# Kernel tuning notes

Measured on AMD Instinct MI355X. Metric: run time of the kernel, lower is better.

## Reference

```python
import jax, jax.numpy as jnp
import numpy as np

NEG_SLOPE = 0.2  # PyG GATConv default negative_slope


def _add_self_loops(edge_index, num_nodes):
    # PyG GATConv add_self_loops=True default
    loop = jnp.arange(num_nodes, dtype=edge_index.dtype)
    src = jnp.concatenate([edge_index[0], loop])
    dst = jnp.concatenate([edge_index[1], loop])
    return src, dst


def _gat_layer(x, src, dst, W, att_src, att_dst, bias, heads, out_ch):
    """One PyG-style GATConv layer (concat=True).
    x: [N, F_in]; W: [F_in, heads*out_ch]; att_*: [heads, out_ch]; bias: [heads*out_ch].
    """
    N = x.shape[0]
    h = (x @ W).reshape(N, heads, out_ch)               # [N, H, C]
    a_src = jnp.einsum('nhc,hc->nh', h, att_src)        # [N, H]
    a_dst = jnp.einsum('nhc,hc->nh', h, att_dst)        # [N, H]
    logits = jax.nn.leaky_relu(a_src[src] + a_dst[dst], NEG_SLOPE)  # [E, H]
    # segment softmax over destination neighborhoods
    m = jax.ops.segment_max(logits, dst, num_segments=N)            # [N, H]
    e = jnp.exp(logits - m[dst])                                     # [E, H]
    s = jax.ops.segment_sum(e, dst, num_segments=N)                  # [N, H]
    alpha = e / s[dst]                                               # [E, H]
    # scatter-aggregate weighted source features
    out = jax.ops.segment_sum(alpha[:, :, None] * h[src], dst, num_segments=N)  # [N, H, C]
    return out.reshape(N, heads * out_ch) + bias


def setup_inputs() -> dict:
    key = jax.random.key(0)
    ks = jax.random.split(key, 10)
    N, E = 50000, 800000
    F_in, HID, H, NC = 128, 64, 4, 10
    x = jax.random.normal(ks[0], (N, F_in), dtype=jnp.float32)
    edge_index = jax.random.randint(ks[1], (2, E), 0, N, dtype=jnp.int64)
    sc1 = 1.0 / np.sqrt(F_in)
    sc2 = 1.0 / np.sqrt(HID * H)
    return {
        'x': x,
        'edge_index': edge_index,
        'W1': jax.random.normal(ks[2], (F_in, H * HID), dtype=jnp.float32) * sc1,
        'att_src1': jax.random.normal(ks[3], (H, HID), dtype=jnp.float32) * sc1,
        'att_dst1': jax.random.normal(ks[4], (H, HID), dtype=jnp.float32) * sc1,
        'b1': jnp.zeros((H * HID,), dtype=jnp.float32),
        'W2': jax.random.normal(ks[5], (H * HID, NC), dtype=jnp.float32) * sc2,
        'att_src2': jax.random.normal(ks[6], (1, NC), dtype=jnp.float32) * sc2,
        'att_dst2': jax.random.normal(ks[7], (1, NC), dtype=jnp.float32) * sc2,
        'b2': jnp.zeros((NC,), dtype=jnp.float32),
    }


def reference(x, edge_index, W1, att_src1, att_dst1, b1, W2, att_src2, att_dst2, b2):
    N = x.shape[0]
    src, dst = _add_self_loops(edge_index, N)
    h = _gat_layer(x, src, dst, W1, att_src1, att_dst1, b1, heads=4, out_ch=64)
    h = jax.nn.elu(h)
    out = _gat_layer(h, src, dst, W2, att_src2, att_dst2, b2, heads=1, out_ch=10)
    return out
```

## Files before the change

kernel.cpp:

```cpp
#include <hip/hip_runtime.h>
#include <hip/hip_fp16.h>
#include <math.h>

#define NEG_SLOPE 0.2f
#define LOG2E 1.44269504088896f

#if __has_builtin(__builtin_amdgcn_exp2f)
#define EXP2(x) __builtin_amdgcn_exp2f(x)
#else
#define EXP2(x) exp2f(x)
#endif

typedef _Float16 half8 __attribute__((ext_vector_type(8)));
typedef float floatx4 __attribute__((ext_vector_type(4)));

#define SRC_TILE_SHIFT 13
#define NTILES 8

__global__ __launch_bounds__(256) void prep1(const float* __restrict__ W1,
                                             half8* __restrict__ Bpack,
                                             int* __restrict__ deg, int N) {
  if (blockIdx.x < 16) {
    int tid = blockIdx.x * 256 + threadIdx.x;
    int l = tid & 63;
    int ksnt = tid >> 6;
    int ks = ksnt & 3;
    int nt = ksnt >> 2;
    int col = nt * 16 + (l & 15);
    int krow = ks * 32 + (l >> 4) * 8;
    half8 v;
#pragma unroll
    for (int j = 0; j < 8; j++) v[j] = (_Float16)W1[(krow + j) * 256 + col];
    Bpack[tid] = v;
  } else {
    int i = (blockIdx.x - 16) * 256 + threadIdx.x;
    if (i < N * NTILES) deg[i] = 0;
  }
}

__global__ __launch_bounds__(256) void phase2(
    const float* __restrict__ x, const half8* __restrict__ Bpack,
    const float* __restrict__ att_s, const float* __restrict__ att_d,
    unsigned char* __restrict__ h1q, float* __restrict__ a1sx,
    float* __restrict__ a1d,
    const int* __restrict__ src, const int* __restrict__ dst,
    int* __restrict__ deg, int* __restrict__ rank,
    int N, int E, int gemmBlocks, int histBlocks) {
  if ((int)blockIdx.x >= gemmBlocks) {
    int b = blockIdx.x - gemmBlocks;
    for (int e = b * 256 + threadIdx.x; e < E; e += histBlocks * 256) {
      int tile = src[e] >> SRC_TILE_SHIFT;
      rank[e] = atomicAdd(deg + dst[e] * NTILES + tile, 1);
    }
    return;
  }
  const int wave = threadIdx.x >> 6, lane = threadIdx.x & 63;
  const int quad = lane >> 4, li = lane & 15;
  const int n0 = (blockIdx.x * 4 + wave) * 16;
  if (n0 >= N) return;
  floatx4 acc[16];
#pragma unroll
  for (int t = 0; t < 16; t++) acc[t] = (floatx4){0.f, 0.f, 0.f, 0.f};
  const float* xrow = x + (size_t)(n0 + li) * 128;
#pragma unroll
  for (int ks = 0; ks < 4; ks++) {
    float4 xa = *(const float4*)(xrow + ks * 32 + quad * 8);
    float4 xb = *(const float4*)(xrow + ks * 32 + quad * 8 + 4);
    half8 a;
    a[0] = (_Float16)xa.x; a[1] = (_Float16)xa.y;
    a[2] = (_Float16)xa.z; a[3] = (_Float16)xa.w;
    a[4] = (_Float16)xb.x; a[5] = (_Float16)xb.y;
    a[6] = (_Float16)xb.z; a[7] = (_Float16)xb.w;
#pragma unroll
    for (int nt = 0; nt < 16; nt++) {
      half8 b = Bpack[(nt * 4 + ks) * 64 + lane];
      acc[nt] = __builtin_amdgcn_mfma_f32_16x16x32_f16(a, b, acc[nt], 0, 0, 0);
    }
  }
#pragma unroll
  for (int r = 0; r < 4; r++) {
    float m = 0.f;
#pragma unroll
    for (int nt = 0; nt < 16; nt++) m = fmaxf(m, fabsf(acc[nt][r]));
#pragma unroll
    for (int off = 8; off > 0; off >>= 1) m = fmaxf(m, __shfl_xor(m, off, 16));
    m = fmaxf(m, 1e-8f);
    float inv = 127.0f / m;
    int node = n0 + quad * 4 + r;
    if (li == 0) a1sx[(size_t)node * 8 + 4] = m * (1.0f / 127.0f);
#pragma unroll
    for (int nt = 0; nt < 16; nt++) {
      h1q[(size_t)node * 256 + nt * 16 + li] =
          (unsigned char)(int)(fmaf(acc[nt][r], inv, 128.5f));
    }
  }
  float as_f[16], ad_f[16];
#pragma unroll
  for (int nt = 0; nt < 16; nt++) {
    as_f[nt] = att_s[nt * 16 + li];
    ad_f[nt] = att_d[nt * 16 + li];
  }
#pragma unroll
  for (int r = 0; r < 4; r++) {
    int node = n0 + quad * 4 + r;
#pragma unroll
    for (int h = 0; h < 4; h++) {
      float vs = 0.f, vd = 0.f;
#pragma unroll
      for (int ntl = 0; ntl < 4; ntl++) {
        int nt = h * 4 + ntl;
        vs = fmaf(acc[nt][r], as_f[nt], vs);
        vd = fmaf(acc[nt][r], ad_f[nt], vd);
      }
#pragma unroll
      for (int off = 8; off > 0; off >>= 1) {
        vs += __shfl_down(vs, off, 16);
        vd += __shfl_down(vd, off, 16);
      }
      if (li == 0) {
        a1sx[(size_t)node * 8 + h] = vs * LOG2E;
        a1d[node * 4 + h] = vd * LOG2E;
      }
    }
  }
}

__global__ void scan_local(const int* __restrict__ deg, int* __restrict__ excl,
                           int* __restrict__ bsum, int N) {
  __shared__ int s[256];
  int i = blockIdx.x * 256 + threadIdx.x;
  int v = 0;
  if (i < N) {
    const int4* dp = (const int4*)(deg + (size_t)i * NTILES);
    int4 c0 = dp[0], c1 = dp[1];
    v = c0.x + c0.y + c0.z + c0.w + c1.x + c1.y + c1.z + c1.w + 1;
  }
  s[threadIdx.x] = v;
  __syncthreads();
  for (int off = 1; off < 256; off <<= 1) {
    int t = (threadIdx.x >= off) ? s[threadIdx.x - off] : 0;
    __syncthreads();
    s[threadIdx.x] += t;
    __syncthreads();
  }
  if (i < N) excl[i] = s[threadIdx.x] - v;
  if (threadIdx.x == 255) bsum[blockIdx.x] = s[255];
}

__global__ void scan_add2(const int* __restrict__ excl, const int* __restrict__ bsum,
                          int* __restrict__ rowptr, int* __restrict__ elist,
                          int N, int nb) {
  __shared__ int s[256];
  int v = (threadIdx.x < nb) ? bsum[threadIdx.x] : 0;
  s[threadIdx.x] = v;
  __syncthreads();
  for (int off = 1; off < 256; off <<= 1) {
    int t = (threadIdx.x >= off) ? s[threadIdx.x - off] : 0;
    __syncthreads();
    s[threadIdx.x] += t;
    __syncthreads();
  }
  __syncthreads();
  int base = (blockIdx.x > 0) ? s[blockIdx.x - 1] : 0;
  int i = blockIdx.x * 256 + threadIdx.x;
  if (i < N) {
    int r = excl[i] + base;
    rowptr[i] = r;
    elist[r] = i;
  }
  if (blockIdx.x == 0 && threadIdx.x == 0) rowptr[N] = s[nb - 1];
}

__global__ void scatter2(const int* __restrict__ src, const int* __restrict__ dst,
                         const int* __restrict__ rank, const int* __restrict__ rowptr,
                         const int* __restrict__ deg, int* __restrict__ elist, int E) {
  int e = blockIdx.x * 256 + threadIdx.x;
  if (e >= E) return;
  int s = src[e];
  int d = dst[e];
  int tile = s >> SRC_TILE_SHIFT;
  const int4* dp = (const int4*)(deg + (size_t)d * NTILES);
  int4 c0 = dp[0], c1 = dp[1];
  int cnt[8] = {c0.x, c0.y, c0.z, c0.w, c1.x, c1.y, c1.z, c1.w};
  int pre = 0;
#pragma unroll
  for (int t = 0; t < 7; t++) pre += (t < tile) ? cnt[t] : 0;
  elist[rowptr[d] + 1 + pre + rank[e]] = s;
}

__global__ __launch_bounds__(256) void agg1_fused(
    const int* __restrict__ rowptr, const int* __restrict__ elist,
    const unsigned char* __restrict__ h1q, const float* __restrict__ a1sx,
    const float* __restrict__ a1d,
    const float* __restrict__ b1, const float* __restrict__ W2,
    const float* __restrict__ as2, const float* __restrict__ ad2,
    __half* __restrict__ h2, int N) {
  __shared__ float w2s[64 * 41];
  __shared__ float cbuf[8][256];
  const int t = threadIdx.x;
  for (int i = t; i < 2560; i += 256) {
    int ch = i / 10, jj = i - ch * 10;
    w2s[(ch >> 2) * 41 + (ch & 3) * 10 + jj] = W2[i];
  }

  const int wave = t >> 6, lane = t & 63;
  const int half = lane >> 5, l32 = lane & 31;
  const int slot = wave * 2 + half;
  const int n = blockIdx.x * 8 + slot;
  const bool act = n < N;
  const int row = act ? rowptr[n] : 0;
  const int deg = act ? rowptr[n + 1] - row : 0;
  const int* el = elist + row;
  const int hidx = l32 >> 3;
  const float adh = act ? a1d[n * 4 + hidx] : 0.f;

  float den = 0.f, T = 0.f;
  float acc[8];
#pragma unroll
  for (int k = 0; k < 8; k++) acc[k] = 0.f;

  int j = 0;
  for (; j + 4 <= deg; j += 4) {
    int ss[4];
    float lv[4], sc[4];
    uint2 qv[4];
#pragma unroll
    for (int u = 0; u < 4; u++) ss[u] = el[j + u];
#pragma unroll
    for (int u = 0; u < 4; u++) {
      const float* mp = a1sx + (size_t)ss[u] * 8;
      lv[u] = mp[hidx];
      sc[u] = mp[4];
      qv[u] = *(const uint2*)(h1q + (size_t)ss[u] * 256 + l32 * 8);
    }
#pragma unroll
    for (int u = 0; u < 4; u++) {
      float l = lv[u] + adh;
      float e = EXP2(fmaxf(l, NEG_SLOPE * l));
      den += e;
      float se = e * sc[u];
      T += se;
      unsigned int a = qv[u].x, b = qv[u].y;
      acc[0] = fmaf((float)(a & 0xffu), se, acc[0]);
      acc[1] = fmaf((float)((a >> 8) & 0xffu), se, acc[1]);
      acc[2] = fmaf((float)((a >> 16) & 0xffu), se, acc[2]);
      acc[3] = fmaf((float)(a >> 24), se, acc[3]);
      acc[4] = fmaf((float)(b & 0xffu), se, acc[4]);
      acc[5] = fmaf((float)((b >> 8) & 0xffu), se, acc[5]);
      acc[6] = fmaf((float)((b >> 16) & 0xffu), se, acc[6]);
      acc[7] = fmaf((float)(b >> 24), se, acc[7]);
    }
  }
  for (; j < deg; j++) {
    int s0 = el[j];
    const float* mp = a1sx + (size_t)s0 * 8;
    float l0 = mp[hidx] + adh;
    float sc0 = mp[4];
    uint2 q0 = *(const uint2*)(h1q + (size_t)s0 * 256 + l32 * 8);
    float e0 = EXP2(fmaxf(l0, NEG_SLOPE * l0));
    den += e0;
    float se = e0 * sc0;
    T += se;
    unsigned int a = q0.x, b = q0.y;
    acc[0] = fmaf((float)(a & 0xffu), se, acc[0]);
    acc[1] = fmaf((float)((a >> 8) & 0xffu), se, acc[1]);
    acc[2] = fmaf((float)((a >> 16) & 0xffu), se, acc[2]);
    acc[3] = fmaf((float)(a >> 24), se, acc[3]);
    acc[4] = fmaf((float)(b & 0xffu), se, acc[4]);
    acc[5] = fmaf((float)((b >> 8) & 0xffu), se, acc[5]);
    acc[6] = fmaf((float)((b >> 16) & 0xffu), se, acc[6]);
    acc[7] = fmaf((float)(b >> 24), se, acc[7]);
  }

  if (act) {
    float inv = 1.0f / den;
    float corr = 128.0f * T;
    float4 v0 = make_float4((acc[0] - corr) * inv, (acc[1] - corr) * inv,
                            (acc[2] - corr) * inv, (acc[3] - corr) * inv);
    float4 v1 = make_float4((acc[4] - corr) * inv, (acc[5] - corr) * inv,
                            (acc[6] - corr) * inv, (acc[7] - corr) * inv);
    *(float4*)&cbuf[slot][l32 * 8] = v0;
    *(float4*)&cbuf[slot][l32 * 8 + 4] = v1;
  }
  __syncthreads();

  float4 bb = *(const float4*)(b1 + lane * 4);
  const float* w0 = w2s + lane * 41;
#pragma unroll
  for (int pp = 0; pp < 2; pp++) {
    int slot2 = wave * 2 + pp;
    int n2 = blockIdx.x * 8 + slot2;
    if (n2 >= N) continue;
    float4 cv = *(const float4*)&cbuf[slot2][lane * 4];
    float c0 = cv.x + bb.x;
    float c1 = cv.y + bb.y;
    float c2 = cv.z + bb.z;
    float c3 = cv.w + bb.w;
    c0 = c0 > 0.f ? c0 : expm1f(c0);
    c1 = c1 > 0.f ? c1 : expm1f(c1);
    c2 = c2 > 0.f ? c2 : expm1f(c2);
    c3 = c3 > 0.f ? c3 : expm1f(c3);
    float p[10];
#pragma unroll
    for (int jj = 0; jj < 10; jj++)
      p[jj] = fmaf(c0, w0[jj],
              fmaf(c1, w0[10 + jj], fmaf(c2, w0[20 + jj], c3 * w0[30 + jj])));
#pragma unroll
    for (int jj = 0; jj < 10; jj++) {
#pragma unroll
      for (int off = 32; off > 0; off >>= 1) p[jj] += __shfl_down(p[jj], off, 64);
    }
    if (lane == 0) {
      float ds = 0.f, dd = 0.f;
#pragma unroll
      for (int jj = 0; jj < 10; jj++) {
        h2[(size_t)n2 * 16 + jj] = __float2half(p[jj]);
        ds = fmaf(p[jj], as2[jj], ds);
        dd = fmaf(p[jj], ad2[jj], dd);
      }
      float* ft = (float*)(h2 + (size_t)n2 * 16);
      ft[5] = ds * LOG2E;
      ft[6] = dd * LOG2E;
    }
  }
}

__global__ __launch_bounds__(256) void agg2_csr(
    const int* __restrict__ rowptr, const int* __restrict__ elist,
    const __half* __restrict__ h2, const float* __restrict__ b2,
    float* __restrict__ out, int N) {
  int wave = threadIdx.x >> 6, lane = threadIdx.x & 63;
  int n = blockIdx.x * 4 + wave;
  if (n >= N) return;
  int row = rowptr[n];
  int deg = rowptr[n + 1] - row;
  const int* el = elist + row;
  const float* hf = (const float*)h2;
  float ad = hf[(size_t)n * 8 + 6];
  int g = lane / 5;
  int c2 = lane - g * 5;
  float den = 0.f, ax = 0.f, ay = 0.f;
  if (g < 12) {
    int jj = g;
    for (; jj + 12 < deg; jj += 24) {
      int sA = el[jj], sB = el[jj + 12];
      float lA = hf[(size_t)sA * 8 + 5] + ad;
      float lB = hf[(size_t)sB * 8 + 5] + ad;
      __half2 hA = *(const __half2*)(h2 + (size_t)sA * 16 + c2 * 2);
      __half2 hB = *(const __half2*)(h2 + (size_t)sB * 16 + c2 * 2);
      float eA = EXP2(fmaxf(lA, NEG_SLOPE * lA));
      float eB = EXP2(fmaxf(lB, NEG_SLOPE * lB));
      den += eA + eB;
      float2 fA = __half22float2(hA);
      float2 fB = __half22float2(hB);
      ax = fmaf(eA, fA.x, fmaf(eB, fB.x, ax));
      ay = fmaf(eA, fA.y, fmaf(eB, fB.y, ay));
    }
    for (; jj < deg; jj += 12) {
      int s = el[jj];
      float l = hf[(size_t)s * 8 + 5] + ad;
      __half2 hv = *(const __half2*)(h2 + (size_t)s * 16 + c2 * 2);
      float ev = EXP2(fmaxf(l, NEG_SLOPE * l));
      den += ev;
      float2 f = __half22float2(hv);
      ax = fmaf(ev, f.x, ax);
      ay = fmaf(ev, f.y, ay);
    }
  }
  ax += __shfl_down(ax, 30, 64);
  ay += __shfl_down(ay, 30, 64);
  den += __shfl_down(den, 30, 64);
  ax += __shfl_down(ax, 10, 64) + __shfl_down(ax, 20, 64);
  ay += __shfl_down(ay, 10, 64) + __shfl_down(ay, 20, 64);
  den += __shfl_down(den, 10, 64) + __shfl_down(den, 20, 64);
  ax += __shfl_down(ax, 5, 64);
  ay += __shfl_down(ay, 5, 64);
  den += __shfl_down(den, 5, 64);
  if (lane < 5) {
    float inv = 1.0f / den;
    float2 bb = *(const float2*)(b2 + lane * 2);
    float2 o = make_float2(fmaf(ax, inv, bb.x), fmaf(ay, inv, bb.y));
    *(float2*)(out + (size_t)n * 10 + lane * 2) = o;
  }
}

extern "C" void kernel_launch(void* const* d_in, const int* in_sizes, int n_in,
                              void* d_out, int out_size, void* d_ws, size_t ws_size,
                              hipStream_t stream) {
  const float* x = (const float*)d_in[0];
  const int* ei = (const int*)d_in[1];
  const float* W1 = (const float*)d_in[2];
  const float* as1 = (const float*)d_in[3];
  const float* ad1 = (const float*)d_in[4];
  const float* b1 = (const float*)d_in[5];
  const float* W2 = (const float*)d_in[6];
  const float* as2 = (const float*)d_in[7];
  const float* ad2 = (const float*)d_in[8];
  const float* b2 = (const float*)d_in[9];
  float* out = (float*)d_out;

  const int N = in_sizes[0] / 128;
  const int E = in_sizes[1] / 2;
  const int* srcp = ei;
  const int* dstp = ei + E;

  char* ws = (char*)d_ws;
  size_t off = 0;
  auto alloc = [&](size_t nbytes) {
    char* p = ws + off;
    off += (nbytes + 255) & ~(size_t)255;
    return p;
  };
  unsigned char* h1q = (unsigned char*)alloc((size_t)N * 256);
  float* a1sx = (float*)alloc((size_t)N * 8 * 4);
  half8* Bpack = (half8*)alloc((size_t)4096 * 16);
  float* a1d = (float*)alloc((size_t)N * 4 * 4);
  __half* h2 = (__half*)alloc((size_t)N * 16 * 2);
  int* deg = (int*)alloc((size_t)N * NTILES * 4);
  int* excl = (int*)alloc((size_t)N * 4);
  int* bsum = (int*)alloc(256 * 4);
  int* rowptr = (int*)alloc((size_t)(N + 1) * 4);
  int* rank = (int*)alloc((size_t)E * 4);
  int* elist = (int*)alloc((size_t)(E + (size_t)N) * 4);

  const int nb = (N + 255) / 256;
  const int nbz = (N * NTILES + 255) / 256;
  const int gemmBlocks = (N / 16 + 3) / 4;
  const int histBlocks = 512;

  prep1<<<16 + nbz, 256, 0, stream>>>(W1, Bpack, deg, N);
  phase2<<<gemmBlocks + histBlocks, 256, 0, stream>>>(
      x, Bpack, as1, ad1, h1q, a1sx, a1d, srcp, dstp, deg, rank, N, E,
      gemmBlocks, histBlocks);
  scan_local<<<nb, 256, 0, stream>>>(deg, excl, bsum, N);
  scan_add2<<<nb, 256, 0, stream>>>(excl, bsum, rowptr, elist, N, nb);
  scatter2<<<(E + 255) / 256, 256, 0, stream>>>(srcp, dstp, rank, rowptr, deg,
                                                elist, E);
  agg1_fused<<<(N + 7) / 8, 256, 0, stream>>>(rowptr, elist, h1q, a1sx, a1d,
                                              b1, W2, as2, ad2, h2, N);
  agg2_csr<<<(N + 3) / 4, 256, 0, stream>>>(rowptr, elist, h2, b2, out, N);
}
```

Baseline: 250.3 us.

## Process layer-1 aggregation in source tiles with grid-wide barrier for L2 reuse

Replaces the per-node agg1 kernel with a persistent 1024-block kernel in which each block handles 56 destination nodes. It walks the 7 source tiles in lockstep across all blocks, using a spin barrier on a global counter so that the tile's h1q rows stay resident in L2. Each block prefetches its slice of the tile before the barrier. It also precomputes per-tile row pointers (rowptr2) in scan_add2, which simplifies scatter2. The cost is more register pressure from 7 groups of accumulators, plus a spin barrier that could stall or time out if not all 1024 blocks are co-resident.

Result: slower. 829.9 us (+231.6%).

```diff
diff --git a/kernel.cpp b/kernel.cpp
--- a/kernel.cpp
+++ b/kernel.cpp
@@ -16,10 +16,14 @@
 
 #define SRC_TILE_SHIFT 13
 #define NTILES 8
+#define NT 7
+#define GROUPS 7
+#define COOP_BLOCKS 1024
 
 __global__ __launch_bounds__(256) void prep1(const float* __restrict__ W1,
                                              half8* __restrict__ Bpack,
-                                             int* __restrict__ deg, int N) {
+                                             int* __restrict__ deg,
+                                             int* __restrict__ bar, int N) {
   if (blockIdx.x < 16) {
     int tid = blockIdx.x * 256 + threadIdx.x;
     int l = tid & 63;
@@ -35,6 +39,7 @@
   } else {
     int i = (blockIdx.x - 16) * 256 + threadIdx.x;
     if (i < N * NTILES) deg[i] = 0;
+    if (i < NT) bar[i] = 0;
   }
 }
 
@@ -148,8 +153,9 @@
 }
 
 __global__ void scan_add2(const int* __restrict__ excl, const int* __restrict__ bsum,
-                          int* __restrict__ rowptr, int* __restrict__ elist,
-                          int N, int nb) {
+                          const int* __restrict__ deg,
+                          int* __restrict__ rowptr, int* __restrict__ rowptr2,
+                          int* __restrict__ elist, int N, int nb) {
   __shared__ int s[256];
   int v = (threadIdx.x < nb) ? bsum[threadIdx.x] : 0;
   s[threadIdx.x] = v;
@@ -167,34 +173,37 @@
     int r = excl[i] + base;
     rowptr[i] = r;
     elist[r] = i;
+    int start = r + 1;
+    int* rp2 = rowptr2 + (size_t)i * 8;
+#pragma unroll
+    for (int tt = 0; tt < NT; ++tt) {
+      rp2[tt] = start;
+      start += deg[(size_t)i * NTILES + tt];
+    }
+    rp2[7] = start;
   }
   if (blockIdx.x == 0 && threadIdx.x == 0) rowptr[N] = s[nb - 1];
 }
 
 __global__ void scatter2(const int* __restrict__ src, const int* __restrict__ dst,
-                         const int* __restrict__ rank, const int* __restrict__ rowptr,
-                         const int* __restrict__ deg, int* __restrict__ elist, int E) {
+                         const int* __restrict__ rank,
+                         const int* __restrict__ rowptr2,
+                         int* __restrict__ elist, int E) {
   int e = blockIdx.x * 256 + threadIdx.x;
   if (e >= E) return;
   int s = src[e];
   int d = dst[e];
   int tile = s >> SRC_TILE_SHIFT;
-  const int4* dp = (const int4*)(deg + (size_t)d * NTILES);
-  int4 c0 = dp[0], c1 = dp[1];
-  int cnt[8] = {c0.x, c0.y, c0.z, c0.w, c1.x, c1.y, c1.z, c1.w};
-  int pre = 0;
-#pragma unroll
-  for (int t = 0; t < 7; t++) pre += (t < tile) ? cnt[t] : 0;
-  elist[rowptr[d] + 1 + pre + rank[e]] = s;
-}
-
-__global__ __launch_bounds__(256) void agg1_fused(
-    const int* __restrict__ rowptr, const int* __restrict__ elist,
+  elist[rowptr2[(size_t)d * 8 + tile] + rank[e]] = s;
+}
+
+__global__ __launch_bounds__(256, 4) void agg1_coop(
+    const int* __restrict__ rowptr2, const int* __restrict__ elist,
     const unsigned char* __restrict__ h1q, const float* __restrict__ a1sx,
     const float* __restrict__ a1d,
     const float* __restrict__ b1, const float* __restrict__ W2,
     const float* __restrict__ as2, const float* __restrict__ ad2,
-    __half* __restrict__ h2, int N) {
+    __half* __restrict__ h2, int* __restrict__ bar, int N) {
   __shared__ float w2s[64 * 41];
   __shared__ float cbuf[8][256];
   const int t = threadIdx.x;
@@ -202,127 +211,174 @@
     int ch = i / 10, jj = i - ch * 10;
     w2s[(ch >> 2) * 41 + (ch & 3) * 10 + jj] = W2[i];
   }
-
   const int wave = t >> 6, lane = t & 63;
   const int half = lane >> 5, l32 = lane & 31;
   const int slot = wave * 2 + half;
-  const int n = blockIdx.x * 8 + slot;
-  const bool act = n < N;
-  const int row = act ? rowptr[n] : 0;
-  const int deg = act ? rowptr[n + 1] - row : 0;
-  const int* el = elist + row;
   const int hidx = l32 >> 3;
-  const float adh = act ? a1d[n * 4 + hidx] : 0.f;
-
-  float den = 0.f, T = 0.f;
-  float acc[8];
-#pragma unroll
-  for (int k = 0; k < 8; k++) acc[k] = 0.f;
-
-  int j = 0;
-  for (; j + 4 <= deg; j += 4) {
-    int ss[4];
-    float lv[4], sc[4];
-    uint2 qv[4];
-#pragma unroll
-    for (int u = 0; u < 4; u++) ss[u] = el[j + u];
-#pragma unroll
-    for (int u = 0; u < 4; u++) {
-      const float* mp = a1sx + (size_t)ss[u] * 8;
-      lv[u] = mp[hidx];
-      sc[u] = mp[4];
-      qv[u] = *(const uint2*)(h1q + (size_t)ss[u] * 256 + l32 * 8);
-    }
-#pragma unroll
-    for (int u = 0; u < 4; u++) {
-      float l = lv[u] + adh;
-      float e = EXP2(fmaxf(l, NEG_SLOPE * l));
-      den += e;
-      float se = e * sc[u];
-      T += se;
-      unsigned int a = qv[u].x, b = qv[u].y;
-      acc[0] = fmaf((float)(a & 0xffu), se, acc[0]);
-      acc[1] = fmaf((float)((a >> 8) & 0xffu), se, acc[1]);
-      acc[2] = fmaf((float)((a >> 16) & 0xffu), se, acc[2]);
-      acc[3] = fmaf((float)(a >> 24), se, acc[3]);
-      acc[4] = fmaf((float)(b & 0xffu), se, acc[4]);
-      acc[5] = fmaf((float)((b >> 8) & 0xffu), se, acc[5]);
-      acc[6] = fmaf((float)((b >> 16) & 0xffu), se, acc[6]);
-      acc[7] = fmaf((float)(b >> 24), se, acc[7]);
-    }
-  }
-  for (; j < deg; j++) {
-    int s0 = el[j];
-    const float* mp = a1sx + (size_t)s0 * 8;
-    float l0 = mp[hidx] + adh;
-    float sc0 = mp[4];
-    uint2 q0 = *(const uint2*)(h1q + (size_t)s0 * 256 + l32 * 8);
-    float e0 = EXP2(fmaxf(l0, NEG_SLOPE * l0));
-    den += e0;
-    float se = e0 * sc0;
-    T += se;
-    unsigned int a = q0.x, b = q0.y;
-    acc[0] = fmaf((float)(a & 0xffu), se, acc[0]);
-    acc[1] = fmaf((float)((a >> 8) & 0xffu), se, acc[1]);
-    acc[2] = fmaf((float)((a >> 16) & 0xffu), se, acc[2]);
-    acc[3] = fmaf((float)(a >> 24), se, acc[3]);
-    acc[4] = fmaf((float)(b & 0xffu), se, acc[4]);
-    acc[5] = fmaf((float)((b >> 8) & 0xffu), se, acc[5]);
-    acc[6] = fmaf((float)((b >> 16) & 0xffu), se, acc[6]);
-    acc[7] = fmaf((float)(b >> 24), se, acc[7]);
-  }
-
-  if (act) {
-    float inv = 1.0f / den;
-    float corr = 128.0f * T;
-    float4 v0 = make_float4((acc[0] - corr) * inv, (acc[1] - corr) * inv,
-                            (acc[2] - corr) * inv, (acc[3] - corr) * inv);
-    float4 v1 = make_float4((acc[4] - corr) * inv, (acc[5] - corr) * inv,
-                            (acc[6] - corr) * inv, (acc[7] - corr) * inv);
-    *(float4*)&cbuf[slot][l32 * 8] = v0;
-    *(float4*)&cbuf[slot][l32 * 8 + 4] = v1;
-  }
-  __syncthreads();
+  const int base = blockIdx.x * (8 * GROUPS);
+  const unsigned char* h1ql = h1q + l32 * 8;
+
+  float den[GROUPS], T[GROUPS], adh[GROUPS], acc[GROUPS][8];
+#pragma unroll
+  for (int g = 0; g < GROUPS; ++g) {
+    den[g] = 0.f;
+    T[g] = 0.f;
+    int ng = base + g * 8 + slot;
+    adh[g] = (ng < N) ? a1d[ng * 4 + hidx] : 0.f;
+#pragma unroll
+    for (int k = 0; k < 8; ++k) acc[g][k] = 0.f;
+  }
+
+#define EDGE1(SV)                                                     \
+  do {                                                                \
+    int _s = (SV);                                                    \
+    const float* _mp = a1sx + (size_t)_s * 8;                         \
+    float _lv = _mp[hidx];                                            \
+    float _sc = _mp[4];                                               \
+    uint2 _q = *(const uint2*)(h1ql + ((size_t)_s << 8));             \
+    float _l = _lv + adh[g];                                          \
+    float _e = EXP2(fmaxf(_l, NEG_SLOPE * _l));                       \
+    den[g] += _e;                                                     \
+    float _se = _e * _sc;                                             \
+    T[g] += _se;                                                      \
+    unsigned _a = _q.x, _b = _q.y;                                    \
+    acc[g][0] = fmaf((float)(_a & 0xffu), _se, acc[g][0]);            \
+    acc[g][1] = fmaf((float)((_a >> 8) & 0xffu), _se, acc[g][1]);     \
+    acc[g][2] = fmaf((float)((_a >> 16) & 0xffu), _se, acc[g][2]);    \
+    acc[g][3] = fmaf((float)(_a >> 24), _se, acc[g][3]);              \
+    acc[g][4] = fmaf((float)(_b & 0xffu), _se, acc[g][4]);            \
+    acc[g][5] = fmaf((float)((_b >> 8) & 0xffu), _se, acc[g][5]);     \
+    acc[g][6] = fmaf((float)((_b >> 16) & 0xffu), _se, acc[g][6]);    \
+    acc[g][7] = fmaf((float)(_b >> 24), _se, acc[g][7]);              \
+  } while (0)
+
+  const size_t Nbytes = (size_t)N << 8;
+  for (int tile = 0; tile < NT; ++tile) {
+    {
+      size_t tb = ((size_t)tile << (SRC_TILE_SHIFT + 8)) +
+                  ((size_t)(blockIdx.x >> 3) << 14) + (size_t)t * 64;
+#pragma unroll
+      for (int k = 0; k < 4; ++k) {
+        size_t a = tb + (size_t)k * 16;
+        if (a < Nbytes) {
+          uint4 v = *(const uint4*)(h1q + a);
+          asm volatile("" ::"v"(v.x), "v"(v.y), "v"(v.z), "v"(v.w));
+        }
+      }
+    }
+    __syncthreads();
+    if (t == 0) {
+      atomicAdd(bar + tile, 1);
+      int sp = 0;
+      while (sp < 20000) {
+        if (__hip_atomic_load(bar + tile, __ATOMIC_RELAXED,
+                              __HIP_MEMORY_SCOPE_AGENT) >= COOP_BLOCKS)
+          break;
+        __builtin_amdgcn_s_sleep(1);
+        ++sp;
+      }
+    }
+    __syncthreads();
+#pragma unroll
+    for (int g = 0; g < GROUPS; ++g) {
+      int ng = base + g * 8 + slot;
+      if (ng >= N) continue;
+      int j = rowptr2[(size_t)ng * 8 + tile];
+      int en = rowptr2[(size_t)ng * 8 + tile + 1];
+      for (; j + 4 <= en; j += 4) {
+        int ss[4];
+        float lv4[4], sc4[4];
+        uint2 qv[4];
+#pragma unroll
+        for (int u = 0; u < 4; ++u) ss[u] = elist[j + u];
+#pragma unroll
+        for (int u = 0; u < 4; ++u) {
+          const float* mp = a1sx + (size_t)ss[u] * 8;
+          lv4[u] = mp[hidx];
+          sc4[u] = mp[4];
+          qv[u] = *(const uint2*)(h1ql + ((size_t)ss[u] << 8));
+        }
+#pragma unroll
+        for (int u = 0; u < 4; ++u) {
+          float l = lv4[u] + adh[g];
+          float e = EXP2(fmaxf(l, NEG_SLOPE * l));
+          den[g] += e;
+          float se = e * sc4[u];
+          T[g] += se;
+          unsigned a = qv[u].x, b = qv[u].y;
+          acc[g][0] = fmaf((float)(a & 0xffu), se, acc[g][0]);
+          acc[g][1] = fmaf((float)((a >> 8) & 0xffu), se, acc[g][1]);
+          acc[g][2] = fmaf((float)((a >> 16) & 0xffu), se, acc[g][2]);
+          acc[g][3] = fmaf((float)(a >> 24), se, acc[g][3]);
+          acc[g][4] = fmaf((float)(b & 0xffu), se, acc[g][4]);
+          acc[g][5] = fmaf((float)((b >> 8) & 0xffu), se, acc[g][5]);
+          acc[g][6] = fmaf((float)((b >> 16) & 0xffu), se, acc[g][6]);
+          acc[g][7] = fmaf((float)(b >> 24), se, acc[g][7]);
+        }
+      }
+      for (; j < en; ++j) EDGE1(elist[j]);
+      if ((ng >> SRC_TILE_SHIFT) == tile) EDGE1(ng);
+    }
+  }
 
   float4 bb = *(const float4*)(b1 + lane * 4);
   const float* w0 = w2s + lane * 41;
 #pragma unroll
-  for (int pp = 0; pp < 2; pp++) {
-    int slot2 = wave * 2 + pp;
-    int n2 = blockIdx.x * 8 + slot2;
-    if (n2 >= N) continue;
-    float4 cv = *(const float4*)&cbuf[slot2][lane * 4];
-    float c0 = cv.x + bb.x;
-    float c1 = cv.y + bb.y;
-    float c2 = cv.z + bb.z;
-    float c3 = cv.w + bb.w;
-    c0 = c0 > 0.f ? c0 : expm1f(c0);
-    c1 = c1 > 0.f ? c1 : expm1f(c1);
-    c2 = c2 > 0.f ? c2 : expm1f(c2);
-    c3 = c3 > 0.f ? c3 : expm1f(c3);
-    float p[10];
-#pragma unroll
-    for (int jj = 0; jj < 10; jj++)
-      p[jj] = fmaf(c0, w0[jj],
-              fmaf(c1, w0[10 + jj], fmaf(c2, w0[20 + jj], c3 * w0[30 + jj])));
-#pragma unroll
-    for (int jj = 0; jj < 10; jj++) {
-#pragma unroll
-      for (int off = 32; off > 0; off >>= 1) p[jj] += __shfl_down(p[jj], off, 64);
-    }
-    if (lane == 0) {
-      float ds = 0.f, dd = 0.f;
+  for (int g = 0; g < GROUPS; ++g) {
+    int nb2 = base + g * 8;
+    if (nb2 >= N) break;
+    int ng = nb2 + slot;
+    if (ng < N) {
+      float inv = 1.0f / den[g];
+      float corr = 128.0f * T[g];
+      float4 v0 = make_float4((acc[g][0] - corr) * inv, (acc[g][1] - corr) * inv,
+                              (acc[g][2] - corr) * inv, (acc[g][3] - corr) * inv);
+      float4 v1 = make_float4((acc[g][4] - corr) * inv, (acc[g][5] - corr) * inv,
+                              (acc[g][6] - corr) * inv, (acc[g][7] - corr) * inv);
+      *(float4*)&cbuf[slot][l32 * 8] = v0;
+      *(float4*)&cbuf[slot][l32 * 8 + 4] = v1;
+    }
+    __syncthreads();
+#pragma unroll
+    for (int pp = 0; pp < 2; pp++) {
+      int slot2 = wave * 2 + pp;
+      int n2 = nb2 + slot2;
+      if (n2 >= N) continue;
+      float4 cv = *(const float4*)&cbuf[slot2][lane * 4];
+      float c0 = cv.x + bb.x;
+      float c1 = cv.y + bb.y;
+      float c2 = cv.z + bb.z;
+      float c3 = cv.w + bb.w;
+      c0 = c0 > 0.f ? c0 : expm1f(c0);
+      c1 = c1 > 0.f ? c1 : expm1f(c1);
+      c2 = c2 > 0.f ? c2 : expm1f(c2);
+      c3 = c3 > 0.f ? c3 : expm1f(c3);
+      float p[10];
+#pragma unroll
+      for (int jj = 0; jj < 10; jj++)
+        p[jj] = fmaf(c0, w0[jj],
+                fmaf(c1, w0[10 + jj], fmaf(c2, w0[20 + jj], c3 * w0[30 + jj])));
 #pragma unroll
       for (int jj = 0; jj < 10; jj++) {
-        h2[(size_t)n2 * 16 + jj] = __float2half(p[jj]);
-        ds = fmaf(p[jj], as2[jj], ds);
-        dd = fmaf(p[jj], ad2[jj], dd);
-      }
-      float* ft = (float*)(h2 + (size_t)n2 * 16);
-      ft[5] = ds * LOG2E;
-      ft[6] = dd * LOG2E;
-    }
-  }
+#pragma unroll
+        for (int off = 32; off > 0; off >>= 1) p[jj] += __shfl_down(p[jj], off, 64);
+      }
+      if (lane == 0) {
+        float ds = 0.f, dd = 0.f;
+#pragma unroll
+        for (int jj = 0; jj < 10; jj++) {
+          h2[(size_t)n2 * 16 + jj] = __float2half(p[jj]);
+          ds = fmaf(p[jj], as2[jj], ds);
+          dd = fmaf(p[jj], ad2[jj], dd);
+        }
+        float* ft = (float*)(h2 + (size_t)n2 * 16);
+        ft[5] = ds * LOG2E;
+        ft[6] = dd * LOG2E;
+      }
+    }
+    __syncthreads();
+  }
+#undef EDGE1
 }
 
 __global__ __launch_bounds__(256) void agg2_csr(
@@ -420,23 +476,24 @@
   int* excl = (int*)alloc((size_t)N * 4);
   int* bsum = (int*)alloc(256 * 4);
   int* rowptr = (int*)alloc((size_t)(N + 1) * 4);
+  int* rowptr2 = (int*)alloc((size_t)N * 8 * 4);
   int* rank = (int*)alloc((size_t)E * 4);
   int* elist = (int*)alloc((size_t)(E + (size_t)N) * 4);
+  int* bar = (int*)alloc(64);
 
   const int nb = (N + 255) / 256;
   const int nbz = (N * NTILES + 255) / 256;
   const int gemmBlocks = (N / 16 + 3) / 4;
   const int histBlocks = 512;
 
-  prep1<<<16 + nbz, 256, 0, stream>>>(W1, Bpack, deg, N);
+  prep1<<<16 + nbz, 256, 0, stream>>>(W1, Bpack, deg, bar, N);
   phase2<<<gemmBlocks + histBlocks, 256, 0, stream>>>(
       x, Bpack, as1, ad1, h1q, a1sx, a1d, srcp, dstp, deg, rank, N, E,
       gemmBlocks, histBlocks);
   scan_local<<<nb, 256, 0, stream>>>(deg, excl, bsum, N);
-  scan_add2<<<nb, 256, 0, stream>>>(excl, bsum, rowptr, elist, N, nb);
-  scatter2<<<(E + 255) / 256, 256, 0, stream>>>(srcp, dstp, rank, rowptr, deg,
-                                                elist, E);
-  agg1_fused<<<(N + 7) / 8, 256, 0, stream>>>(rowptr, elist, h1q, a1sx, a1d,
-                                              b1, W2, as2, ad2, h2, N);
+  scan_add2<<<nb, 256, 0, stream>>>(excl, bsum, deg, rowptr, rowptr2, elist, N, nb);
+  scatter2<<<(E + 255) / 256, 256, 0, stream>>>(srcp, dstp, rank, rowptr2, elist, E);
+  agg1_coop<<<COOP_BLOCKS, 256, 0, stream>>>(rowptr2, elist, h1q, a1sx, a1d,
+                                             b1, W2, as2, ad2, h2, bar, N);
   agg2_csr<<<(N + 3) / 4, 256, 0, stream>>>(rowptr, elist, h2, b2, out, N);
 }
```
